# Performance work log

Measured on AMD Instinct MI355X. Metric: run time of the kernel, lower is better.

The kernel has to match this reference:

```python
import jax, jax.numpy as jnp
import numpy as np

NEG_INF = -9e15
ALPHA = 0.2  # attention leaky_relu slope


def _gat_layer(h, adj_mask, W, a1, a2):
    # h: [N, Fin], W: [Fin, D], a1/a2: [D]
    Wh = h @ W                                   # [N, D]
    f1 = Wh @ a1                                 # [N]
    f2 = Wh @ a2                                 # [N]
    e = jax.nn.leaky_relu(f1[:, None] + f2[None, :], ALPHA)  # [N, N]
    scores = jnp.where(adj_mask, e, NEG_INF)
    att = jax.nn.softmax(scores, axis=-1)        # row-normalized over neighbors
    return att @ Wh                              # [N, D]


def setup_inputs() -> dict:
    key = jax.random.key(0)
    ks = jax.random.split(key, 12)
    N, Fin, H, D, C = 4096, 512, 8, 64, 64
    s = 0.1
    x = jax.random.normal(ks[0], (N, Fin), jnp.float32)
    adj = jax.random.randint(ks[1], (N, N), 0, 2, jnp.int32)
    W = jax.random.normal(ks[2], (H, Fin, D), jnp.float32) * s
    a1 = jax.random.normal(ks[3], (H, D), jnp.float32) * s
    a2 = jax.random.normal(ks[4], (H, D), jnp.float32) * s
    Wo = jax.random.normal(ks[5], (H * D, C), jnp.float32) * s
    ao1 = jax.random.normal(ks[6], (C,), jnp.float32) * s
    ao2 = jax.random.normal(ks[7], (C,), jnp.float32) * s
    W1 = jax.random.normal(ks[8], (512, N), jnp.float32) * 0.01  # nn.Linear(N, 512)
    b1 = jnp.zeros((512,), jnp.float32)
    W2 = jax.random.normal(ks[9], (256, 512), jnp.float32) * 0.04  # nn.Linear(512, 256)
    b2 = jnp.zeros((256,), jnp.float32)
    return {"x": x, "adj": adj, "W": W, "a1": a1, "a2": a2,
            "Wo": Wo, "ao1": ao1, "ao2": ao2,
            "W1": W1, "b1": b1, "W2": W2, "b2": b2}


def reference(x, adj, W, a1, a2, Wo, ao1, ao2, W1, b1, W2, b2):
    mask = adj > 0                                    # [N, N]
    # multi-head dense attention, concat=True -> ELU per head
    heads = jax.vmap(lambda Wk, a1k, a2k: _gat_layer(x, mask, Wk, a1k, a2k))(W, a1, a2)  # [H, N, D]
    h = jax.nn.elu(heads).transpose(1, 0, 2).reshape(x.shape[0], -1)  # [N, H*D]
    # output attention layer, concat=False (no inner ELU), then outer ELU
    out = jax.nn.elu(_gat_layer(h, mask, Wo, ao1, ao2))  # [N, C]
    out = jax.nn.log_softmax(out, axis=0)                # over nodes (dim=0)
    # MLP head on transposed features: [C, N] -> [C, 512] -> [C, 256]
    y = jax.nn.leaky_relu(out.T @ W1.T + b1, 0.1)
    y = y @ W2.T + b2
    return y
```

## Files before the change

### kernel.cpp

```cpp
#include <hip/hip_runtime.h>
#include <hip/hip_bf16.h>
#include <math.h>


#define N_NODES 4096
#define FIN 512
#define NHEAD 8
#define DHEAD 64
#define NCLS 64

typedef unsigned short u16;
typedef unsigned long long u64;
typedef __attribute__((ext_vector_type(8))) short bf16x8;
typedef __attribute__((ext_vector_type(4))) float f32x4;

__device__ __forceinline__ float lrelu02(float x) { return x > 0.f ? x : 0.2f * x; }
__device__ __forceinline__ u16 bf16u(float x) {
    __hip_bfloat16 h = __float2bfloat16(x);
    return __builtin_bit_cast(unsigned short, h);
}
__device__ __forceinline__ f32x4 mfma16(bf16x8 a, bf16x8 b, f32x4 c) {
    return __builtin_amdgcn_mfma_f32_16x16x32_bf16(a, b, c, 0, 0, 0);
}
__device__ __forceinline__ unsigned fkey(float f) {
    unsigned u = __builtin_bit_cast(unsigned, f);
    return (u & 0x80000000u) ? ~u : (u | 0x80000000u);
}
__device__ __forceinline__ float funkey(unsigned k) {
    unsigned u = (k & 0x80000000u) ? (k ^ 0x80000000u) : ~k;
    return __builtin_bit_cast(float, u);
}

__global__ __launch_bounds__(256) void prep(
    const int* __restrict__ adj, u64* __restrict__ mbA, unsigned* __restrict__ gmk,
    const float* __restrict__ x, u16* __restrict__ xB,
    const float* __restrict__ W1, u16* __restrict__ W1B,
    const float* __restrict__ W, const float* __restrict__ Wo,
    u16* __restrict__ WBt, u16* __restrict__ WoBt) {
    __shared__ alignas(16) u16 T[64][72];
    const int bid = blockIdx.x, t = threadIdx.x;
    if (bid < 4096) {
        int i = bid * 256 + t;
        const float* s;
        u16* d;
        if (i < N_NODES * FIN / 4) { s = x; d = xB; }
        else { i -= N_NODES * FIN / 4; s = W1; d = W1B; }
        float4 v = ((const float4*)s)[i];
        ushort4 o = {bf16u(v.x), bf16u(v.y), bf16u(v.z), bf16u(v.w)};
        ((ushort4*)d)[i] = o;
    } else if (bid < 8192) {
        if (bid == 4096 && t < 16) gmk[t] = 0u;
        const int lane = t & 63;
        const int task = (bid - 4096) * 4 + (t >> 6);
        const int g = task >> 6, jt = task & 63;
        const int r = lane & 15, kq = lane >> 4;
        const int* ap = adj + (size_t)(g * 16 + r) * N_NODES + jt * 64 + kq * 8;
        int4 c0 = *(const int4*)(ap);
        int4 c1 = *(const int4*)(ap + 4);
        int4 c2 = *(const int4*)(ap + 32);
        int4 c3 = *(const int4*)(ap + 36);
        u64 myw = 0;
        #pragma unroll
        for (int w = 0; w < 16; ++w) {
            const int hf = w >> 3, i = w & 7;
            int val;
            if (hf == 0) val = (i < 4) ? ((const int*)&c0)[i & 3] : ((const int*)&c1)[i & 3];
            else         val = (i < 4) ? ((const int*)&c2)[i & 3] : ((const int*)&c3)[i & 3];
            u64 bal = __ballot(val > 0);
            if (lane == w) myw = bal;
        }
        if (lane < 16) mbA[((size_t)g * 64 + jt) * 16 + lane] = myw;
    } else {
        int idx = bid - 8192;
        int y = idx >> 3, xb = idx & 7;
        const float* src = (y < 8) ? W + (size_t)y * FIN * DHEAD : Wo;
        u16* d = (y < 8) ? WBt + (size_t)y * DHEAD * FIN : WoBt;
        const int j0 = xb * 64;
        const int row = t & 63, g = t >> 6;
        #pragma unroll
        for (int k = 0; k < 16; k += 4) {
            float4 v = *(const float4*)(src + (size_t)(j0 + row) * 64 + g * 16 + k);
            T[g * 16 + k + 0][row] = bf16u(v.x);
            T[g * 16 + k + 1][row] = bf16u(v.y);
            T[g * 16 + k + 2][row] = bf16u(v.z);
            T[g * 16 + k + 3][row] = bf16u(v.w);
        }
        __syncthreads();
        const int dd = t >> 2, jc = (t & 3) * 16;
        *(uint4*)(d + (size_t)dd * FIN + j0 + jc) = *(const uint4*)&T[dd][jc];
        *(uint4*)(d + (size_t)dd * FIN + j0 + jc + 8) = *(const uint4*)&T[dd][jc + 8];
    }
}

__global__ __launch_bounds__(256) void gemm_fused(
    const u16* __restrict__ A, int lda, const u16* __restrict__ Bt, int ldb,
    const float* __restrict__ a1a, const float* __restrict__ a2a,
    u16* __restrict__ WhBT, float* __restrict__ f1o, float* __restrict__ f2o,
    unsigned* __restrict__ gmk, int K) {
    __shared__ alignas(16) u16 T[64][72];
    const int t = threadIdx.x, lane = t & 63, wv = t >> 6;
    const int c16 = lane & 15, kg = lane >> 4;
    const int h = blockIdx.x;
    const int bm = blockIdx.y * 64;
    const u16* Ap = A + (size_t)(bm + wv * 16 + c16) * lda + kg * 8;
    const u16* Bp = Bt + (size_t)(h * 64 + c16) * ldb + kg * 8;
    f32x4 acc[4] = {};
    #pragma unroll 4
    for (int k0 = 0; k0 < K; k0 += 32) {
        bf16x8 a = *(const bf16x8*)(Ap + k0);
        #pragma unroll
        for (int ct = 0; ct < 4; ++ct) {
            bf16x8 b = *(const bf16x8*)(Bp + (size_t)ct * 16 * ldb + k0);
            acc[ct] = mfma16(a, b, acc[ct]);
        }
    }
    float a1v[4], a2v[4];
    #pragma unroll
    for (int ct = 0; ct < 4; ++ct) {
        a1v[ct] = a1a[h * 64 + ct * 16 + c16];
        a2v[ct] = a2a[h * 64 + ct * 16 + c16];
    }
    float mx = -1e30f;
    #pragma unroll
    for (int r = 0; r < 4; ++r) {
        float s1 = 0.f, s2 = 0.f;
        int rl = wv * 16 + kg * 4 + r;
        #pragma unroll
        for (int ct = 0; ct < 4; ++ct) {
            float v = acc[ct][r];
            s1 = fmaf(v, a1v[ct], s1);
            s2 = fmaf(v, a2v[ct], s2);
            T[ct * 16 + c16][rl] = bf16u(v);
        }
        #pragma unroll
        for (int off = 1; off < 16; off <<= 1) {
            s1 += __shfl_xor(s1, off, 64);
            s2 += __shfl_xor(s2, off, 64);
        }
        if (c16 == 0) {
            f1o[(size_t)h * N_NODES + bm + rl] = s1;
            f2o[(size_t)h * N_NODES + bm + rl] = s2;
        }
        mx = fmaxf(mx, s2);
    }
    mx = fmaxf(mx, __shfl_xor(mx, 16, 64));
    mx = fmaxf(mx, __shfl_xor(mx, 32, 64));
    if (lane == 0) atomicMax(&gmk[h], fkey(mx));
    __syncthreads();
    const int dd = t >> 2, jc = (t & 3) * 16;
    u16* dst = WhBT + (size_t)(h * 64 + dd) * N_NODES + bm;
    *(uint4*)(dst + jc) = *(const uint4*)&T[dd][jc];
    *(uint4*)(dst + jc + 8) = *(const uint4*)&T[dd][jc + 8];
}

__global__ void coefk(const float* __restrict__ f1, const float* __restrict__ f2,
                      const unsigned* __restrict__ gmk, float2* __restrict__ rowc,
                      float2* __restrict__ uv) {
    int h = blockIdx.y;
    int i = blockIdx.x * 256 + threadIdx.x;
    float g = funkey(gmk[h]);
    float a = f1[(size_t)h * N_NODES + i];
    float s = a + g;
    float M = lrelu02(s);
    rowc[(size_t)h * N_NODES + i] = make_float2(__expf(s - M), __expf(0.2f * s - M));
    float b = f2[(size_t)h * N_NODES + i] - g;
    uv[(size_t)h * N_NODES + i] = make_float2(__expf(b), __expf(0.2f * b));
}

template <int NH, int MT, int JSPLIT, int LJS>
__global__ __launch_bounds__(256) void attn_v6(
    const u16* __restrict__ WhB, const float2* __restrict__ uv,
    const float2* __restrict__ rowc, const u64* __restrict__ mbA,
    float* __restrict__ outp, float* __restrict__ denP) {
    constexpr int NJT = 64 / JSPLIT;
    constexpr int OC = (NH == 8) ? 512 : 64;
    const int t = threadIdx.x, lane = t & 63;
    const int gw = __builtin_amdgcn_readfirstlane(blockIdx.x * 4 + (t >> 6));
    int h, ib, js;
    if (NH == 8) { h = gw & 7; int rest = gw >> 3; js = rest & (JSPLIT - 1); ib = rest >> LJS; }
    else { h = 0; js = gw & (JSPLIT - 1); ib = gw >> LJS; }
    const int i0 = ib * (MT * 16);
    const int g0 = i0 >> 4;
    const int jt0 = js * NJT;
    const int kg = lane >> 4, c16 = lane & 15;

    const float* uvf = (const float*)(uv + (size_t)h * N_NODES);
    const float2* rcp = rowc + (size_t)h * N_NODES;

    float Aq[MT], Bq[MT], den[MT];
    #pragma unroll
    for (int mt = 0; mt < MT; ++mt) {
        float2 rc = rcp[i0 + mt * 16 + c16];
        Aq[mt] = rc.x; Bq[mt] = rc.y; den[mt] = 0.f;
    }
    const u16* bp[4];
    #pragma unroll
    for (int ct = 0; ct < 4; ++ct)
        bp[ct] = WhB + ((size_t)h * 64 + ct * 16 + c16) * N_NODES + kg * 8;

    f32x4 acc[MT][4] = {};

    for (int it = 0; it < NJT; ++it) {
        const int jt = jt0 + it;
        const float* up = uvf + (size_t)(jt * 64 + kg * 8) * 2;
        float4 u0[4], u1[4];
        #pragma unroll
        for (int k = 0; k < 4; ++k) {
            u0[k] = *(const float4*)(up + k * 4);
            u1[k] = *(const float4*)(up + 64 + k * 4);
        }
        bf16x8 bfr[4][2];
        #pragma unroll
        for (int ct = 0; ct < 4; ++ct) {
            bfr[ct][0] = *(const bf16x8*)(bp[ct] + (size_t)jt * 64);
            bfr[ct][1] = *(const bf16x8*)(bp[ct] + (size_t)jt * 64 + 32);
        }
        #pragma unroll
        for (int mt = 0; mt < MT; ++mt) {
            const u64* mw = mbA + ((size_t)(g0 + mt) * 64 + jt) * 16;
            unsigned pk[8];
            #pragma unroll
            for (int hf = 0; hf < 2; ++hf) {
                #pragma unroll
                for (int k = 0; k < 4; ++k) {
                    float4 q = hf ? u1[k] : u0[k];
                    u64 w0 = mw[hf * 8 + 2 * k];
                    u64 w1 = mw[hf * 8 + 2 * k + 1];
                    unsigned l0 = __builtin_amdgcn_readfirstlane((unsigned)w0);
                    unsigned h0 = __builtin_amdgcn_readfirstlane((unsigned)(w0 >> 32));
                    unsigned l1 = __builtin_amdgcn_readfirstlane((unsigned)w1);
                    unsigned h1 = __builtin_amdgcn_readfirstlane((unsigned)(w1 >> 32));
                    u64 ws0 = ((u64)h0 << 32) | l0;
                    u64 ws1 = ((u64)h1 << 32) | l1;
                    float t0 = fmaxf(Aq[mt] * q.x, Bq[mt] * q.y);
                    float t1 = fmaxf(Aq[mt] * q.z, Bq[mt] * q.w);
                    float p0, p1;
                    asm("v_cndmask_b32 %0, 0, %1, %2" : "=v"(p0) : "v"(t0), "s"(ws0));
                    asm("v_cndmask_b32 %0, 0, %1, %2" : "=v"(p1) : "v"(t1), "s"(ws1));
                    den[mt] += p0 + p1;
                    unsigned pkd;
                    asm("v_cvt_pk_bf16_f32 %0, %1, %2" : "=v"(pkd) : "v"(p0), "v"(p1));
                    pk[hf * 4 + k] = pkd;
                }
            }
            union { unsigned d[4]; bf16x8 v; } ua, ub;
            #pragma unroll
            for (int k = 0; k < 4; ++k) { ua.d[k] = pk[k]; ub.d[k] = pk[4 + k]; }
            #pragma unroll
            for (int ct = 0; ct < 4; ++ct) {
                acc[mt][ct] = mfma16(ua.v, bfr[ct][0], acc[mt][ct]);
                acc[mt][ct] = mfma16(ub.v, bfr[ct][1], acc[mt][ct]);
            }
        }
    }

    #pragma unroll
    for (int mt = 0; mt < MT; ++mt) {
        den[mt] += __shfl_xor(den[mt], 16, 64);
        den[mt] += __shfl_xor(den[mt], 32, 64);
    }
    float* denDst = (NH == 8) ? denP + (size_t)js * (8 * N_NODES) + (size_t)h * N_NODES
                              : denP + (size_t)js * N_NODES;
    if (lane < 16) {
        #pragma unroll
        for (int mt = 0; mt < MT; ++mt) denDst[i0 + mt * 16 + lane] = den[mt];
    }
    float* dst = outp + (size_t)js * N_NODES * OC + h * 64;
    #pragma unroll
    for (int mt = 0; mt < MT; ++mt)
        #pragma unroll
        for (int ct = 0; ct < 4; ++ct)
            #pragma unroll
            for (int r = 0; r < 4; ++r)
                dst[(size_t)(i0 + mt * 16 + kg * 4 + r) * OC + ct * 16 + c16] = acc[mt][ct][r];
}

__global__ __launch_bounds__(256) void combine8(
    const float* __restrict__ part, const float* __restrict__ denp,
    u16* __restrict__ hB) {
    const int t4 = (blockIdx.x * 256 + threadIdx.x) * 4;
    const int i = t4 >> 9, c = t4 & 511, h = c >> 6;
    float4 p0 = *(const float4*)(part + t4);
    float4 p1 = *(const float4*)(part + (size_t)N_NODES * 512 + t4);
    float d = denp[h * N_NODES + i] + denp[8 * N_NODES + h * N_NODES + i];
    float inv = d > 0.f ? 1.f / d : 0.f;
    float v[4] = {(p0.x + p1.x) * inv, (p0.y + p1.y) * inv,
                  (p0.z + p1.z) * inv, (p0.w + p1.w) * inv};
    ushort4 o;
    #pragma unroll
    for (int k = 0; k < 4; ++k) {
        float e = v[k] > 0.f ? v[k] : expm1f(v[k]);
        ((u16*)&o)[k] = bf16u(e);
    }
    *(ushort4*)(hB + t4) = o;
}

__global__ __launch_bounds__(256) void combine1T(
    const float* __restrict__ part1, const float* __restrict__ den1,
    float* __restrict__ attoutT) {
    __shared__ float T[64][65];
    const int b = blockIdx.x, t = threadIdx.x;
    const int r0 = b * 64;
    const int rl = t >> 2, cg = (t & 3) * 16;
    const int row = r0 + rl;
    float d = 0.f;
    #pragma unroll
    for (int js = 0; js < 8; ++js) d += den1[(size_t)js * N_NODES + row];
    float inv = d > 0.f ? 1.f / d : 0.f;
    float s[16] = {};
    #pragma unroll
    for (int js = 0; js < 8; ++js) {
        const float* p = part1 + (size_t)js * N_NODES * 64 + (size_t)row * 64 + cg;
        #pragma unroll
        for (int k = 0; k < 16; k += 4) {
            float4 v = *(const float4*)(p + k);
            s[k] += v.x; s[k + 1] += v.y; s[k + 2] += v.z; s[k + 3] += v.w;
        }
    }
    #pragma unroll
    for (int k = 0; k < 16; ++k) {
        float e = s[k] * inv;
        T[rl][cg + k] = e > 0.f ? e : expm1f(e);
    }
    __syncthreads();
    const int c = t >> 2, seg = (t & 3) * 16;
    #pragma unroll
    for (int k = 0; k < 16; k += 4) {
        float4 v = {T[seg + k][c], T[seg + k + 1][c], T[seg + k + 2][c], T[seg + k + 3][c]};
        *(float4*)(attoutT + (size_t)c * N_NODES + r0 + seg + k) = v;
    }
}

__global__ __launch_bounds__(256) void lsm_row(const float* __restrict__ aT,
                                               u16* __restrict__ lsT) {
    int c = blockIdx.x, t = threadIdx.x;
    const float* row = aT + (size_t)c * N_NODES;
    __shared__ float r[256];
    float m = -1e30f;
    for (int i = t * 4; i < N_NODES; i += 1024) {
        float4 v = *(const float4*)(row + i);
        m = fmaxf(fmaxf(fmaxf(m, v.x), fmaxf(v.y, v.z)), v.w);
    }
    r[t] = m;
    __syncthreads();
    for (int s = 128; s; s >>= 1) {
        if (t < s) r[t] = fmaxf(r[t], r[t + s]);
        __syncthreads();
    }
    m = r[0];
    __syncthreads();
    float sum = 0.f;
    for (int i = t * 4; i < N_NODES; i += 1024) {
        float4 v = *(const float4*)(row + i);
        sum += __expf(v.x - m) + __expf(v.y - m) + __expf(v.z - m) + __expf(v.w - m);
    }
    r[t] = sum;
    __syncthreads();
    for (int s = 128; s; s >>= 1) {
        if (t < s) r[t] += r[t + s];
        __syncthreads();
    }
    float lse = m + __logf(r[0]);
    for (int i = t * 4; i < N_NODES; i += 1024) {
        float4 v = *(const float4*)(row + i);
        ushort4 o = {bf16u(v.x - lse), bf16u(v.y - lse), bf16u(v.z - lse), bf16u(v.w - lse)};
        *(ushort4*)(lsT + (size_t)c * N_NODES + i) = o;
    }
}

__global__ __launch_bounds__(256) void mlp1_mfma(
    const u16* __restrict__ lsT, const u16* __restrict__ W1B,
    float* __restrict__ part) {
    const int t = threadIdx.x, lane = t & 63, wv = t >> 6;
    const int c16 = lane & 15, kg = lane >> 4;
    const int ks = blockIdx.x & 15;
    const int bn = (blockIdx.x >> 4) * 64;
    const int kb = ks * 256;
    const u16* Ap = lsT + (size_t)(wv * 16 + c16) * N_NODES + kb + kg * 8;
    const u16* Bp = W1B + (size_t)(bn + c16) * N_NODES + kb + kg * 8;
    f32x4 acc[4] = {};
    #pragma unroll
    for (int k0 = 0; k0 < 256; k0 += 32) {
        bf16x8 a = *(const bf16x8*)(Ap + k0);
        #pragma unroll
        for (int ct = 0; ct < 4; ++ct) {
            bf16x8 b = *(const bf16x8*)(Bp + (size_t)ct * 16 * N_NODES + k0);
            acc[ct] = mfma16(a, b, acc[ct]);
        }
    }
    float* dst = part + (size_t)ks * 64 * 512;
    #pragma unroll
    for (int ct = 0; ct < 4; ++ct)
        #pragma unroll
        for (int r = 0; r < 4; ++r)
            dst[(size_t)(wv * 16 + kg * 4 + r) * 512 + bn + ct * 16 + c16] = acc[ct][r];
}

__global__ __launch_bounds__(256) void mlp2f(
    const float* __restrict__ part, const float* __restrict__ b1,
    const float* __restrict__ W2, const float* __restrict__ b2,
    float* __restrict__ out) {
    __shared__ alignas(16) float row[512];
    const int c = blockIdx.x, t = threadIdx.x;
    #pragma unroll
    for (int half = 0; half < 2; ++half) {
        int o = t + half * 256;
        float s = 0.f;
        #pragma unroll
        for (int ks = 0; ks < 16; ++ks)
            s += part[(size_t)ks * 32768 + (size_t)c * 512 + o];
        s += b1[o];
        row[o] = s > 0.f ? s : 0.1f * s;
    }
    __syncthreads();
    float acc = 0.f;
    #pragma unroll 4
    for (int o = 0; o < 512; o += 4) {
        float4 w4 = *(const float4*)(W2 + (size_t)t * 512 + o);
        float4 r4 = *(const float4*)(&row[o]);
        acc += w4.x * r4.x + w4.y * r4.y + w4.z * r4.z + w4.w * r4.w;
    }
    out[(size_t)c * 256 + t] = acc + b2[t];
}

extern "C" void kernel_launch(void* const* d_in, const int* in_sizes, int n_in,
                              void* d_out, int out_size, void* d_ws, size_t ws_size,
                              hipStream_t stream) {
    const float* x   = (const float*)d_in[0];
    const int*   adj = (const int*)d_in[1];
    const float* W   = (const float*)d_in[2];
    const float* a1  = (const float*)d_in[3];
    const float* a2  = (const float*)d_in[4];
    const float* Wo  = (const float*)d_in[5];
    const float* ao1 = (const float*)d_in[6];
    const float* ao2 = (const float*)d_in[7];
    const float* W1  = (const float*)d_in[8];
    const float* b1  = (const float*)d_in[9];
    const float* W2  = (const float*)d_in[10];
    const float* b2  = (const float*)d_in[11];
    float* out = (float*)d_out;

    char* ws = (char*)d_ws;
    size_t off = 0;
    auto alloc = [&](size_t bytes) {
        void* p = ws + off;
        off += (bytes + 255) & ~(size_t)255;
        return p;
    };
    u64*     mbA    = (u64*)alloc((size_t)256 * 64 * 16 * 8);
    u16*     xB     = (u16*)alloc((size_t)N_NODES * FIN * 2);
    u16*     WBt    = (u16*)alloc((size_t)NHEAD * DHEAD * FIN * 2);
    u16*     WoBt   = (u16*)alloc((size_t)DHEAD * FIN * 2);
    u16*     W1B    = (u16*)alloc((size_t)512 * N_NODES * 2);
    u16*     WhB    = (u16*)alloc((size_t)NHEAD * DHEAD * N_NODES * 2);
    u16*     WhoB   = (u16*)alloc((size_t)DHEAD * N_NODES * 2);
    u16*     hB     = (u16*)alloc((size_t)N_NODES * 512 * 2);
    float*   part8  = (float*)alloc((size_t)2 * N_NODES * 512 * 4);
    float*   den8   = (float*)alloc((size_t)2 * 8 * N_NODES * 4);
    float*   f1b    = (float*)alloc((size_t)9 * N_NODES * 4);
    float*   f2b    = (float*)alloc((size_t)9 * N_NODES * 4);
    unsigned* gmk   = (unsigned*)alloc(16 * 4);
    float2*  rowc   = (float2*)alloc((size_t)9 * N_NODES * 8);
    float2*  uvb    = (float2*)alloc((size_t)9 * N_NODES * 8);
    char*  ov      = (char*)part8;
    float* part1   = (float*)(ov);
    float* den1    = (float*)(ov + ((size_t)8 << 20));
    float* attoutT = (float*)(ov + ((size_t)9 << 20));
    u16*   lsT     = (u16*)(ov + ((size_t)10 << 20));
    float* part    = (float*)(ov + ((size_t)11 << 20));
    (void)ws_size; (void)in_sizes; (void)n_in; (void)out_size;

    prep<<<8264, 256, 0, stream>>>(adj, mbA, gmk, x, xB, W1, W1B, W, Wo, WBt, WoBt);
    gemm_fused<<<dim3(8, 64), 256, 0, stream>>>(xB, FIN, WBt, FIN, a1, a2,
                                                WhB, f1b, f2b, gmk, FIN);
    coefk<<<dim3(16, 8), 256, 0, stream>>>(f1b, f2b, gmk, rowc, uvb);
    attn_v6<8, 2, 2, 1><<<512, 256, 0, stream>>>(WhB, uvb, rowc, mbA, part8, den8);
    combine8<<<N_NODES * 512 / 4 / 256, 256, 0, stream>>>(part8, den8, hB);
    gemm_fused<<<dim3(1, 64), 256, 0, stream>>>(hB, 512, WoBt, FIN, ao1, ao2,
                                                WhoB, f1b + (size_t)8 * N_NODES,
                                                f2b + (size_t)8 * N_NODES, gmk + 8, FIN);
    coefk<<<dim3(16, 1), 256, 0, stream>>>(f1b + (size_t)8 * N_NODES,
                                           f2b + (size_t)8 * N_NODES, gmk + 8,
                                           rowc + (size_t)8 * N_NODES,
                                           uvb + (size_t)8 * N_NODES);
    attn_v6<1, 1, 8, 3><<<512, 256, 0, stream>>>(
        WhoB, uvb + (size_t)8 * N_NODES, rowc + (size_t)8 * N_NODES, mbA, part1, den1);
    combine1T<<<64, 256, 0, stream>>>(part1, den1, attoutT);
    lsm_row<<<64, 256, 0, stream>>>(attoutT, lsT);
    mlp1_mfma<<<128, 256, 0, stream>>>(lsT, W1B, part);
    mlp2f<<<64, 256, 0, stream>>>(part, b1, W2, b2, out);
}
```

Before: 239.3 us.

## Raise attention split-K, store bf16 partials, group blocks by head

The first-layer attention kernel now splits the neighbor dimension 8 ways instead of 2, and the output layer 16 ways instead of 8, so both launch many more blocks. Partial outputs are written as bf16 instead of fp32, and the combine kernels sum the larger number of partials. Blocks are remapped so that all waves in a block work on the same head, which should improve cache reuse of that head's Wh. The gain in occupancy comes at the cost of more partial data to write and reduce, and of extra rounding error from bf16 partial sums.

```diff
diff --git a/kernel.cpp b/kernel.cpp
--- a/kernel.cpp
+++ b/kernel.cpp
@@ -18,6 +18,10 @@
 __device__ __forceinline__ u16 bf16u(float x) {
     __hip_bfloat16 h = __float2bfloat16(x);
     return __builtin_bit_cast(unsigned short, h);
+}
+__device__ __forceinline__ float b2f(u16 v) {
+    unsigned u = (unsigned)v << 16;
+    return __builtin_bit_cast(float, u);
 }
 __device__ __forceinline__ f32x4 mfma16(bf16x8 a, bf16x8 b, f32x4 c) {
     return __builtin_amdgcn_mfma_f32_16x16x32_bf16(a, b, c, 0, 0, 0);
@@ -171,14 +175,22 @@
 __global__ __launch_bounds__(256) void attn_v6(
     const u16* __restrict__ WhB, const float2* __restrict__ uv,
     const float2* __restrict__ rowc, const u64* __restrict__ mbA,
-    float* __restrict__ outp, float* __restrict__ denP) {
+    u16* __restrict__ outp, float* __restrict__ denP) {
     constexpr int NJT = 64 / JSPLIT;
     constexpr int OC = (NH == 8) ? 512 : 64;
     const int t = threadIdx.x, lane = t & 63;
-    const int gw = __builtin_amdgcn_readfirstlane(blockIdx.x * 4 + (t >> 6));
     int h, ib, js;
-    if (NH == 8) { h = gw & 7; int rest = gw >> 3; js = rest & (JSPLIT - 1); ib = rest >> LJS; }
-    else { h = 0; js = gw & (JSPLIT - 1); ib = gw >> LJS; }
+    if (NH == 8) {
+        h = blockIdx.x & 7;
+        const int wid = __builtin_amdgcn_readfirstlane((blockIdx.x >> 3) * 4 + (t >> 6));
+        js = wid & (JSPLIT - 1);
+        ib = wid >> LJS;
+    } else {
+        h = 0;
+        const int wid = __builtin_amdgcn_readfirstlane(blockIdx.x * 4 + (t >> 6));
+        js = wid & (JSPLIT - 1);
+        ib = wid >> LJS;
+    }
     const int i0 = ib * (MT * 16);
     const int g0 = i0 >> 4;
     const int jt0 = js * NJT;
@@ -265,38 +277,43 @@
         #pragma unroll
         for (int mt = 0; mt < MT; ++mt) denDst[i0 + mt * 16 + lane] = den[mt];
     }
-    float* dst = outp + (size_t)js * N_NODES * OC + h * 64;
+    u16* dst = outp + (size_t)js * N_NODES * OC + h * 64;
     #pragma unroll
     for (int mt = 0; mt < MT; ++mt)
         #pragma unroll
         for (int ct = 0; ct < 4; ++ct)
             #pragma unroll
             for (int r = 0; r < 4; ++r)
-                dst[(size_t)(i0 + mt * 16 + kg * 4 + r) * OC + ct * 16 + c16] = acc[mt][ct][r];
+                dst[(size_t)(i0 + mt * 16 + kg * 4 + r) * OC + ct * 16 + c16] =
+                    bf16u(acc[mt][ct][r]);
 }
 
 __global__ __launch_bounds__(256) void combine8(
-    const float* __restrict__ part, const float* __restrict__ denp,
+    const u16* __restrict__ part, const float* __restrict__ denp,
     u16* __restrict__ hB) {
     const int t4 = (blockIdx.x * 256 + threadIdx.x) * 4;
     const int i = t4 >> 9, c = t4 & 511, h = c >> 6;
-    float4 p0 = *(const float4*)(part + t4);
-    float4 p1 = *(const float4*)(part + (size_t)N_NODES * 512 + t4);
-    float d = denp[h * N_NODES + i] + denp[8 * N_NODES + h * N_NODES + i];
+    float s[4] = {0.f, 0.f, 0.f, 0.f};
+    float d = 0.f;
+    #pragma unroll
+    for (int js = 0; js < 8; ++js) {
+        ushort4 p = *(const ushort4*)(part + (size_t)js * N_NODES * 512 + t4);
+        s[0] += b2f(p.x); s[1] += b2f(p.y); s[2] += b2f(p.z); s[3] += b2f(p.w);
+        d += denp[(size_t)js * (8 * N_NODES) + h * N_NODES + i];
+    }
     float inv = d > 0.f ? 1.f / d : 0.f;
-    float v[4] = {(p0.x + p1.x) * inv, (p0.y + p1.y) * inv,
-                  (p0.z + p1.z) * inv, (p0.w + p1.w) * inv};
     ushort4 o;
     #pragma unroll
     for (int k = 0; k < 4; ++k) {
-        float e = v[k] > 0.f ? v[k] : expm1f(v[k]);
+        float v = s[k] * inv;
+        float e = v > 0.f ? v : expm1f(v);
         ((u16*)&o)[k] = bf16u(e);
     }
     *(ushort4*)(hB + t4) = o;
 }
 
 __global__ __launch_bounds__(256) void combine1T(
-    const float* __restrict__ part1, const float* __restrict__ den1,
+    const u16* __restrict__ part1, const float* __restrict__ den1,
     float* __restrict__ attoutT) {
     __shared__ float T[64][65];
     const int b = blockIdx.x, t = threadIdx.x;
@@ -305,16 +322,17 @@
     const int row = r0 + rl;
     float d = 0.f;
     #pragma unroll
-    for (int js = 0; js < 8; ++js) d += den1[(size_t)js * N_NODES + row];
+    for (int js = 0; js < 16; ++js) d += den1[(size_t)js * N_NODES + row];
     float inv = d > 0.f ? 1.f / d : 0.f;
     float s[16] = {};
     #pragma unroll
-    for (int js = 0; js < 8; ++js) {
-        const float* p = part1 + (size_t)js * N_NODES * 64 + (size_t)row * 64 + cg;
+    for (int js = 0; js < 16; ++js) {
+        const u16* p = part1 + (size_t)js * N_NODES * 64 + (size_t)row * 64 + cg;
         #pragma unroll
         for (int k = 0; k < 16; k += 4) {
-            float4 v = *(const float4*)(p + k);
-            s[k] += v.x; s[k + 1] += v.y; s[k + 2] += v.z; s[k + 3] += v.w;
+            ushort4 v = *(const ushort4*)(p + k);
+            s[k] += b2f(v.x); s[k + 1] += b2f(v.y);
+            s[k + 2] += b2f(v.z); s[k + 3] += b2f(v.w);
         }
     }
     #pragma unroll
@@ -455,15 +473,15 @@
     u16*     WhB    = (u16*)alloc((size_t)NHEAD * DHEAD * N_NODES * 2);
     u16*     WhoB   = (u16*)alloc((size_t)DHEAD * N_NODES * 2);
     u16*     hB     = (u16*)alloc((size_t)N_NODES * 512 * 2);
-    float*   part8  = (float*)alloc((size_t)2 * N_NODES * 512 * 4);
-    float*   den8   = (float*)alloc((size_t)2 * 8 * N_NODES * 4);
+    u16*     part8  = (u16*)alloc((size_t)8 * N_NODES * 512 * 2);
+    float*   den8   = (float*)alloc((size_t)8 * 8 * N_NODES * 4);
     float*   f1b    = (float*)alloc((size_t)9 * N_NODES * 4);
     float*   f2b    = (float*)alloc((size_t)9 * N_NODES * 4);
     unsigned* gmk   = (unsigned*)alloc(16 * 4);
     float2*  rowc   = (float2*)alloc((size_t)9 * N_NODES * 8);
     float2*  uvb    = (float2*)alloc((size_t)9 * N_NODES * 8);
     char*  ov      = (char*)part8;
-    float* part1   = (float*)(ov);
+    u16*   part1   = (u16*)(ov);
     float* den1    = (float*)(ov + ((size_t)8 << 20));
     float* attoutT = (float*)(ov + ((size_t)9 << 20));
     u16*   lsT     = (u16*)(ov + ((size_t)10 << 20));
@@ -474,7 +492,7 @@
     gemm_fused<<<dim3(8, 64), 256, 0, stream>>>(xB, FIN, WBt, FIN, a1, a2,
                                                 WhB, f1b, f2b, gmk, FIN);
     coefk<<<dim3(16, 8), 256, 0, stream>>>(f1b, f2b, gmk, rowc, uvb);
-    attn_v6<8, 2, 2, 1><<<512, 256, 0, stream>>>(WhB, uvb, rowc, mbA, part8, den8);
+    attn_v6<8, 2, 8, 3><<<2048, 256, 0, stream>>>(WhB, uvb, rowc, mbA, part8, den8);
     combine8<<<N_NODES * 512 / 4 / 256, 256, 0, stream>>>(part8, den8, hB);
     gemm_fused<<<dim3(1, 64), 256, 0, stream>>>(hB, 512, WoBt, FIN, ao1, ao2,
                                                 WhoB, f1b + (size_t)8 * N_NODES,
@@ -483,7 +501,7 @@
                                            f2b + (size_t)8 * N_NODES, gmk + 8,
                                            rowc + (size_t)8 * N_NODES,
                                            uvb + (size_t)8 * N_NODES);
-    attn_v6<1, 1, 8, 3><<<512, 256, 0, stream>>>(
+    attn_v6<1, 1, 16, 4><<<1024, 256, 0, stream>>>(
         WhoB, uvb + (size_t)8 * N_NODES, rowc + (size_t)8 * N_NODES, mbA, part1, den1);
     combine1T<<<64, 256, 0, stream>>>(part1, den1, attoutT);
     lsm_row<<<64, 256, 0, stream>>>(attoutT, lsT);
```

Measured after the change: 234.8 us. Within noise of the previous version (-1.9%).
